# Kernel optimization log

Hardware: AMD Instinct MI355X
Metric: run time of the kernel (lower is better)

Reference implementation:

```python
import jax, jax.numpy as jnp
import numpy as np

# Constants matching init_kwargs (block=1, min_==min_ext, max_==max_ext -> deterministic path)
MIN_ = 26214   # bottom-k pixels -> background seeds
MAX_ = 26214   # top-k pixels    -> foreground seeds
KSZ = 3        # dilation kernel (ones) == 3x3 max-pool, SAME padding
IGNORE = -255  # seg_ignore_idx


def _dilate(m):
    # m: (b, h, w) binary int32. kornia dilation with ones kernel == max-pool ksz, stride 1, SAME.
    return jax.lax.reduce_window(m, jnp.int32(0), jax.lax.max,
                                 window_dimensions=(1, KSZ, KSZ),
                                 window_strides=(1, 1, 1),
                                 padding='SAME')


def setup_inputs() -> dict:
    key = jax.random.key(0)
    x = jax.random.normal(key, (128, 1, 512, 512), dtype=jnp.float32)
    return {"x": x}


def reference(x) -> jnp.ndarray:
    b, d, h, w = x.shape  # d == 1
    hw = h * w
    t = x.reshape(b, hw)
    idx = jnp.argsort(t, axis=1)            # ascending, per sample
    rows = jnp.arange(b)[:, None]

    # Foreground: top MAX_ activations, then dilate
    fg = jnp.zeros((b, hw), jnp.int32).at[rows, idx[:, hw - MAX_:]].set(1)
    fg = _dilate(fg.reshape(b, h, w)).reshape(b, hw)

    # Background: bottom MIN_ activations, then dilate
    bg = jnp.zeros((b, hw), jnp.int32).at[rows, idx[:, :MIN_]].set(1)
    bg = _dilate(bg.reshape(b, h, w)).reshape(b, hw)

    # Drop pixels claimed by both
    overlap = (fg + bg) == 2
    fg = jnp.where(overlap, 0, fg)
    bg = jnp.where(overlap, 0, bg)

    seed = jnp.full((b, hw), IGNORE, dtype=jnp.int32)
    seed = jnp.where(fg == 1, 1, seed)
    seed = jnp.where(bg == 1, 0, seed)
    return seed.reshape(b, h, w)
```

## Files before the change

### kernel.cpp

```cpp
#include <hip/hip_runtime.h>
#include <hip/hip_bf16.h>


#define HW      262144
#define NROW    128
#define R1_RANK 26213u
#define R2_RANK 235930u
#define NBIN    8192
#define CAP     8192
#define LCAP    1024
#define CBLK    2048

__device__ __forceinline__ unsigned f2u(float f) {
    unsigned b = __float_as_uint(f);
    return b ^ ((b >> 31) ? 0xFFFFFFFFu : 0x80000000u);
}

__global__ __launch_bounds__(256) void k_hist(const float* __restrict__ x,
                                              unsigned* __restrict__ hist) {
    __shared__ unsigned lh[NBIN];
    for (int i = threadIdx.x; i < NBIN; i += 256) lh[i] = 0;
    __syncthreads();
    int row = blockIdx.x >> 3;
    int chunk = blockIdx.x & 7;
    const float4* p = (const float4*)(x + (size_t)row * HW + (size_t)chunk * 32768);
    for (int it = 0; it < 32; ++it) {
        float4 v = p[it * 256 + threadIdx.x];
        atomicAdd(&lh[f2u(v.x) >> 19], 1u);
        atomicAdd(&lh[f2u(v.y) >> 19], 1u);
        atomicAdd(&lh[f2u(v.z) >> 19], 1u);
        atomicAdd(&lh[f2u(v.w) >> 19], 1u);
    }
    __syncthreads();
    unsigned* gh = hist + (size_t)row * NBIN;
    for (int i = threadIdx.x; i < NBIN; i += 256) {
        unsigned c = lh[i];
        if (c) atomicAdd(&gh[i], c);
    }
}

__global__ __launch_bounds__(256) void k_findbin(const unsigned* __restrict__ hist,
                                                 unsigned* __restrict__ meta) {
    int row = blockIdx.x;
    const unsigned* h = hist + (size_t)row * NBIN;
    __shared__ unsigned psum[256];
    __shared__ unsigned excl[257];
    int base = threadIdx.x * 32;
    unsigned s = 0;
    for (int i = 0; i < 32; ++i) s += h[base + i];
    psum[threadIdx.x] = s;
    __syncthreads();
    if (threadIdx.x == 0) {
        unsigned a = 0;
        for (int t = 0; t < 256; ++t) { excl[t] = a; a += psum[t]; }
        excl[256] = a;
    }
    __syncthreads();
    for (int side = 0; side < 2; ++side) {
        unsigned R = side ? R2_RANK : R1_RANK;
        if (excl[threadIdx.x] <= R && R < excl[threadIdx.x + 1]) {
            unsigned a = excl[threadIdx.x];
            for (int i = 0; i < 32; ++i) {
                unsigned c = h[base + i];
                if (R < a + c) { meta[row * 4 + side * 2] = base + i;
                                 meta[row * 4 + side * 2 + 1] = R - a; break; }
                a += c;
            }
        }
    }
}

__global__ __launch_bounds__(256) void k_collect(const float* __restrict__ x,
                                                 const unsigned* __restrict__ meta,
                                                 unsigned* __restrict__ cnt,
                                                 unsigned long long* __restrict__ cand) {
    __shared__ unsigned long long buf0[CBLK];
    __shared__ unsigned long long buf1[CBLK];
    __shared__ unsigned bcnt[2];
    __shared__ unsigned gbase[2];
    if (threadIdx.x < 2) bcnt[threadIdx.x] = 0;
    __syncthreads();

    size_t ebase = (size_t)blockIdx.x * CBLK;
    int row = (int)(ebase >> 18);
    unsigned bin1 = meta[row * 4 + 0];
    unsigned bin2 = meta[row * 4 + 2];
    const float4* p = (const float4*)(x + ebase);
    #pragma unroll
    for (int j = 0; j < 2; ++j) {
        int t4 = j * 256 + threadIdx.x;
        float4 v = p[t4];
        float vv[4] = {v.x, v.y, v.z, v.w};
        unsigned eidx = (unsigned)((ebase + (size_t)t4 * 4) & (HW - 1));
        #pragma unroll
        for (int k = 0; k < 4; ++k) {
            unsigned u = f2u(vv[k]);
            unsigned bin = u >> 19;
            unsigned long long key = (((unsigned long long)u) << 32) | (eidx + k);
            if (bin == bin1) buf0[atomicAdd(&bcnt[0], 1u)] = key;
            if (bin == bin2) buf1[atomicAdd(&bcnt[1], 1u)] = key;
        }
    }
    __syncthreads();
    if (threadIdx.x < 2)
        gbase[threadIdx.x] = atomicAdd(&cnt[row * 2 + threadIdx.x], bcnt[threadIdx.x]);
    __syncthreads();
    unsigned n0 = bcnt[0], n1 = bcnt[1];
    unsigned long long* c0 = cand + ((size_t)(row * 2 + 0)) * CAP;
    unsigned long long* c1 = cand + ((size_t)(row * 2 + 1)) * CAP;
    for (unsigned i = threadIdx.x; i < n0; i += 256) {
        unsigned slot = gbase[0] + i;
        if (slot < CAP) c0[slot] = buf0[i];
    }
    for (unsigned i = threadIdx.x; i < n1; i += 256) {
        unsigned slot = gbase[1] + i;
        if (slot < CAP) c1[slot] = buf1[i];
    }
}

__global__ __launch_bounds__(256) void k_select(const unsigned* __restrict__ meta,
                                                const unsigned* __restrict__ cnt,
                                                const unsigned long long* __restrict__ cand,
                                                unsigned* __restrict__ thr) {
    int row = blockIdx.x >> 1, side = blockIdx.x & 1;
    unsigned m = cnt[row * 2 + side]; if (m > CAP) m = CAP;
    unsigned r = meta[row * 4 + side * 2 + 1];
    const unsigned long long* ck = cand + ((size_t)(row * 2 + side)) * CAP;

    __shared__ unsigned h2[NBIN];
    __shared__ unsigned psum[256];
    __shared__ unsigned excl[257];
    __shared__ unsigned long long list[LCAP];
    __shared__ unsigned listCnt, subbin_s, rprime_s;
    for (int i = threadIdx.x; i < NBIN; i += 256) h2[i] = 0;
    if (threadIdx.x == 0) listCnt = 0;
    __syncthreads();
    for (unsigned i = threadIdx.x; i < m; i += 256) {
        unsigned u = (unsigned)(ck[i] >> 32);
        atomicAdd(&h2[(u >> 6) & (NBIN - 1)], 1u);
    }
    __syncthreads();
    int base = threadIdx.x * 32;
    unsigned s = 0;
    for (int i = 0; i < 32; ++i) s += h2[base + i];
    psum[threadIdx.x] = s;
    __syncthreads();
    if (threadIdx.x == 0) {
        unsigned a = 0;
        for (int t = 0; t < 256; ++t) { excl[t] = a; a += psum[t]; }
        excl[256] = a;
    }
    __syncthreads();
    if (excl[threadIdx.x] <= r && r < excl[threadIdx.x + 1]) {
        unsigned a = excl[threadIdx.x];
        for (int i = 0; i < 32; ++i) {
            unsigned c = h2[base + i];
            if (r < a + c) { subbin_s = (unsigned)(base + i); rprime_s = r - a; break; }
            a += c;
        }
    }
    __syncthreads();
    unsigned sb = subbin_s, rp = rprime_s;
    for (unsigned i = threadIdx.x; i < m; i += 256) {
        unsigned long long k = ck[i];
        if ((((unsigned)(k >> 32)) >> 6 & (NBIN - 1)) == sb) {
            unsigned slot = atomicAdd(&listCnt, 1u);
            if (slot < LCAP) list[slot] = k;
        }
    }
    __syncthreads();
    unsigned lm = listCnt; if (lm > LCAP) lm = LCAP;
    for (unsigned i = threadIdx.x; i < lm; i += 256) {
        unsigned long long ki = list[i];
        unsigned c = 0;
        for (unsigned j = 0; j < lm; ++j) c += (list[j] < ki);
        if (c == rp) {
            thr[row * 4 + side * 2]     = (unsigned)(ki >> 32);
            thr[row * 4 + side * 2 + 1] = (unsigned)ki;
        }
    }
}

__global__ __launch_bounds__(256) void k_seed(const float* __restrict__ x,
                                              const unsigned* __restrict__ thr,
                                              int* __restrict__ out) {
    int row = blockIdx.z;
    int tx0 = blockIdx.x * 32, ty0 = blockIdx.y * 32;
    __shared__ unsigned char code[34 * 36];
    unsigned T1 = thr[row * 4 + 0], C1 = thr[row * 4 + 1];
    unsigned T2 = thr[row * 4 + 2], C2 = thr[row * 4 + 3];
    const float* xr = x + (size_t)row * HW;
    for (int t = threadIdx.x; t < 34 * 34; t += 256) {
        int ly = t / 34, lx = t % 34;
        int gy = ty0 + ly - 1, gx = tx0 + lx - 1;
        unsigned char c = 0;
        if (gx >= 0 && gx < 512 && gy >= 0 && gy < 512) {
            unsigned idx = (unsigned)(gy * 512 + gx);
            unsigned u = f2u(xr[idx]);
            bool bg = (u < T1) || (u == T1 && idx <= C1);
            bool fg = (u > T2) || (u == T2 && idx >= C2);
            c = (unsigned char)((bg ? 1 : 0) | (fg ? 2 : 0));
        }
        code[ly * 36 + lx] = c;
    }
    __syncthreads();
    int lx = threadIdx.x & 31;
    int ly0 = (threadIdx.x >> 5) * 4;
    #define OR3(r) ((unsigned)(code[(r) * 36 + lx] | code[(r) * 36 + lx + 1] | code[(r) * 36 + lx + 2]))
    unsigned c0 = OR3(ly0), c1 = OR3(ly0 + 1);
    for (int k = 0; k < 4; ++k) {
        unsigned c2 = OR3(ly0 + k + 2);
        unsigned mm = c0 | c1 | c2;
        bool bgd = mm & 1, fgd = mm & 2;
        int o = ((bgd ^ fgd) != 0) ? (fgd ? 1 : 0) : -255;
        out[(size_t)row * HW + (size_t)(ty0 + ly0 + k) * 512 + (tx0 + lx)] = o;
        c0 = c1; c1 = c2;
    }
    #undef OR3
}

extern "C" void kernel_launch(void* const* d_in, const int* in_sizes, int n_in,
                              void* d_out, int out_size, void* d_ws, size_t ws_size,
                              hipStream_t stream) {
    const float* x = (const float*)d_in[0];
    int* out = (int*)d_out;

    char* ws = (char*)d_ws;
    unsigned* hist = (unsigned*)ws;
    unsigned* cnt  = (unsigned*)(ws + (size_t)NROW * NBIN * 4);
    unsigned* meta = (unsigned*)(ws + (size_t)NROW * NBIN * 4 + 1024);
    unsigned* thr  = (unsigned*)(ws + (size_t)NROW * NBIN * 4 + 3072);
    unsigned long long* cand =
        (unsigned long long*)(ws + (size_t)NROW * NBIN * 4 + 8192);

    hipMemsetAsync(d_ws, 0, (size_t)NROW * NBIN * 4 + 1024, stream);

    k_hist<<<NROW * 8, 256, 0, stream>>>(x, hist);
    k_findbin<<<NROW, 256, 0, stream>>>(hist, meta);
    k_collect<<<(NROW * HW) / CBLK, 256, 0, stream>>>(x, meta, cnt, cand);
    k_select<<<NROW * 2, 256, 0, stream>>>(meta, cnt, cand, thr);
    k_seed<<<dim3(16, 16, NROW), 256, 0, stream>>>(x, thr, out);
}
```

Before: 392.0 us.

## Pack histogram bins into 16-bit halves and shrink collect shared buffers

The histogram kernel now packs two 16-bit bin counters per shared word, which halves LDS use, and moves to 512 threads with a software-prefetched load loop. The collect kernel moves to 4096-element blocks with 512 threads and much smaller shared candidate buffers, spilling to global atomics when a buffer overflows. The aim is higher occupancy from less LDS per block, plus fewer blocks. The risks are 16-bit counter overflow if one bin in a chunk gets more than 65535 hits (at most 32768 here, so safe), and a slow global-atomic path if candidates are dense.

```diff
diff --git a/kernel.cpp b/kernel.cpp
--- a/kernel.cpp
+++ b/kernel.cpp
@@ -9,33 +9,41 @@
 #define NBIN    8192
 #define CAP     8192
 #define LCAP    1024
-#define CBLK    2048
+#define CBLK    4096
+#define BUFCAP  1024
 
 __device__ __forceinline__ unsigned f2u(float f) {
     unsigned b = __float_as_uint(f);
     return b ^ ((b >> 31) ? 0xFFFFFFFFu : 0x80000000u);
 }
 
-__global__ __launch_bounds__(256) void k_hist(const float* __restrict__ x,
+__global__ __launch_bounds__(512) void k_hist(const float* __restrict__ x,
                                               unsigned* __restrict__ hist) {
-    __shared__ unsigned lh[NBIN];
-    for (int i = threadIdx.x; i < NBIN; i += 256) lh[i] = 0;
+    __shared__ unsigned lh[NBIN / 2];
+    for (int i = threadIdx.x; i < NBIN / 2; i += 512) lh[i] = 0;
     __syncthreads();
     int row = blockIdx.x >> 3;
     int chunk = blockIdx.x & 7;
     const float4* p = (const float4*)(x + (size_t)row * HW + (size_t)chunk * 32768);
-    for (int it = 0; it < 32; ++it) {
-        float4 v = p[it * 256 + threadIdx.x];
-        atomicAdd(&lh[f2u(v.x) >> 19], 1u);
-        atomicAdd(&lh[f2u(v.y) >> 19], 1u);
-        atomicAdd(&lh[f2u(v.z) >> 19], 1u);
-        atomicAdd(&lh[f2u(v.w) >> 19], 1u);
+    float4 v = p[threadIdx.x];
+    #pragma unroll 4
+    for (int it = 0; it < 16; ++it) {
+        float4 cur = v;
+        if (it < 15) v = p[(it + 1) * 512 + threadIdx.x];
+        unsigned b0 = f2u(cur.x) >> 19, b1 = f2u(cur.y) >> 19;
+        unsigned b2 = f2u(cur.z) >> 19, b3 = f2u(cur.w) >> 19;
+        atomicAdd(&lh[b0 >> 1], (b0 & 1) ? 65536u : 1u);
+        atomicAdd(&lh[b1 >> 1], (b1 & 1) ? 65536u : 1u);
+        atomicAdd(&lh[b2 >> 1], (b2 & 1) ? 65536u : 1u);
+        atomicAdd(&lh[b3 >> 1], (b3 & 1) ? 65536u : 1u);
     }
     __syncthreads();
     unsigned* gh = hist + (size_t)row * NBIN;
-    for (int i = threadIdx.x; i < NBIN; i += 256) {
-        unsigned c = lh[i];
-        if (c) atomicAdd(&gh[i], c);
+    for (int i = threadIdx.x; i < NBIN / 2; i += 512) {
+        unsigned w = lh[i];
+        unsigned lo = w & 0xFFFFu, hi = w >> 16;
+        if (lo) atomicAdd(&gh[2 * i], lo);
+        if (hi) atomicAdd(&gh[2 * i + 1], hi);
     }
 }
 
@@ -70,12 +78,12 @@
     }
 }
 
-__global__ __launch_bounds__(256) void k_collect(const float* __restrict__ x,
+__global__ __launch_bounds__(512) void k_collect(const float* __restrict__ x,
                                                  const unsigned* __restrict__ meta,
                                                  unsigned* __restrict__ cnt,
                                                  unsigned long long* __restrict__ cand) {
-    __shared__ unsigned long long buf0[CBLK];
-    __shared__ unsigned long long buf1[CBLK];
+    __shared__ unsigned long long buf0[BUFCAP];
+    __shared__ unsigned long long buf1[BUFCAP];
     __shared__ unsigned bcnt[2];
     __shared__ unsigned gbase[2];
     if (threadIdx.x < 2) bcnt[threadIdx.x] = 0;
@@ -85,10 +93,12 @@
     int row = (int)(ebase >> 18);
     unsigned bin1 = meta[row * 4 + 0];
     unsigned bin2 = meta[row * 4 + 2];
+    unsigned long long* c0 = cand + ((size_t)(row * 2 + 0)) * CAP;
+    unsigned long long* c1 = cand + ((size_t)(row * 2 + 1)) * CAP;
     const float4* p = (const float4*)(x + ebase);
     #pragma unroll
     for (int j = 0; j < 2; ++j) {
-        int t4 = j * 256 + threadIdx.x;
+        int t4 = j * 512 + threadIdx.x;
         float4 v = p[t4];
         float vv[4] = {v.x, v.y, v.z, v.w};
         unsigned eidx = (unsigned)((ebase + (size_t)t4 * 4) & (HW - 1));
@@ -97,22 +107,29 @@
             unsigned u = f2u(vv[k]);
             unsigned bin = u >> 19;
             unsigned long long key = (((unsigned long long)u) << 32) | (eidx + k);
-            if (bin == bin1) buf0[atomicAdd(&bcnt[0], 1u)] = key;
-            if (bin == bin2) buf1[atomicAdd(&bcnt[1], 1u)] = key;
-        }
-    }
-    __syncthreads();
-    if (threadIdx.x < 2)
-        gbase[threadIdx.x] = atomicAdd(&cnt[row * 2 + threadIdx.x], bcnt[threadIdx.x]);
-    __syncthreads();
-    unsigned n0 = bcnt[0], n1 = bcnt[1];
-    unsigned long long* c0 = cand + ((size_t)(row * 2 + 0)) * CAP;
-    unsigned long long* c1 = cand + ((size_t)(row * 2 + 1)) * CAP;
-    for (unsigned i = threadIdx.x; i < n0; i += 256) {
+            if (bin == bin1) {
+                unsigned s = atomicAdd(&bcnt[0], 1u);
+                if (s < BUFCAP) buf0[s] = key;
+                else { unsigned g = atomicAdd(&cnt[row * 2 + 0], 1u); if (g < CAP) c0[g] = key; }
+            }
+            if (bin == bin2) {
+                unsigned s = atomicAdd(&bcnt[1], 1u);
+                if (s < BUFCAP) buf1[s] = key;
+                else { unsigned g = atomicAdd(&cnt[row * 2 + 1], 1u); if (g < CAP) c1[g] = key; }
+            }
+        }
+    }
+    __syncthreads();
+    unsigned n0 = bcnt[0] < BUFCAP ? bcnt[0] : BUFCAP;
+    unsigned n1 = bcnt[1] < BUFCAP ? bcnt[1] : BUFCAP;
+    if (threadIdx.x == 0) gbase[0] = atomicAdd(&cnt[row * 2 + 0], n0);
+    if (threadIdx.x == 1) gbase[1] = atomicAdd(&cnt[row * 2 + 1], n1);
+    __syncthreads();
+    for (unsigned i = threadIdx.x; i < n0; i += 512) {
         unsigned slot = gbase[0] + i;
         if (slot < CAP) c0[slot] = buf0[i];
     }
-    for (unsigned i = threadIdx.x; i < n1; i += 256) {
+    for (unsigned i = threadIdx.x; i < n1; i += 512) {
         unsigned slot = gbase[1] + i;
         if (slot < CAP) c1[slot] = buf1[i];
     }
@@ -235,9 +252,9 @@
 
     hipMemsetAsync(d_ws, 0, (size_t)NROW * NBIN * 4 + 1024, stream);
 
-    k_hist<<<NROW * 8, 256, 0, stream>>>(x, hist);
+    k_hist<<<NROW * 8, 512, 0, stream>>>(x, hist);
     k_findbin<<<NROW, 256, 0, stream>>>(hist, meta);
-    k_collect<<<(NROW * HW) / CBLK, 256, 0, stream>>>(x, meta, cnt, cand);
+    k_collect<<<(NROW * HW) / CBLK, 512, 0, stream>>>(x, meta, cnt, cand);
     k_select<<<NROW * 2, 256, 0, stream>>>(meta, cnt, cand, thr);
     k_seed<<<dim3(16, 16, NROW), 256, 0, stream>>>(x, thr, out);
 }
```

Result: faster. 383.8 us (-2.1%).
